# Kernel tuning notes

Measured on AMD Instinct MI355X. Metric: run time of the kernel, lower is better.

Reference implementation:

```python
import jax, jax.numpy as jnp
import numpy as np

B, S, H = 64, 2048, 1024
NEG = -1e10


def setup_inputs() -> dict:
    key = jax.random.key(0)
    k1, k2, k3, k4, k5, k6 = jax.random.split(key, 6)
    scale = 1.0 / np.sqrt(2 * H)
    return {
        "decoder_hidden": jax.random.normal(k1, (B, H), dtype=jnp.float32),
        "encoder_outputs": jax.random.normal(k2, (B, S, H), dtype=jnp.float32),
        "mask": jax.random.randint(k3, (B, S), 0, 2, dtype=jnp.int32),
        "W_attn": jax.random.normal(k4, (2 * H, H), dtype=jnp.float32) * scale,
        "b_attn": jax.random.normal(k5, (H,), dtype=jnp.float32) * scale,
        "v_w": jax.random.normal(k6, (H,), dtype=jnp.float32) * (1.0 / np.sqrt(H)),
    }


def reference(decoder_hidden, encoder_outputs, mask, W_attn, b_attn, v_w):
    # concat((dec_rep, enc), -1) @ W_attn == dec @ W_attn[:H] + enc @ W_attn[H:]
    Wd, We = W_attn[:H], W_attn[H:]
    dec_proj = decoder_hidden @ Wd            # [B, H]
    enc_proj = jnp.einsum('bsh,hk->bsk', encoder_outputs, We)  # [B, S, H]
    energy = jnp.tanh(dec_proj[:, None, :] + enc_proj + b_attn)  # [B, S, H]
    attention = jnp.einsum('bsh,h->bs', energy, v_w)             # [B, S]
    attention = jnp.where(mask == 1, NEG, attention)
    return jax.nn.softmax(attention, axis=1)
```

## Files before the change

### kernel.cpp

```cpp
#include <hip/hip_runtime.h>
#include <hip/hip_bf16.h>
#include <stdint.h>

#define HD   1024
#define BB   64
#define SS   2048
#define MT   (BB*SS)
#define NEGV -10000000000.0f

typedef __attribute__((ext_vector_type(8))) short bf16x8;
typedef __attribute__((ext_vector_type(4))) float f32x4;
typedef __attribute__((ext_vector_type(4))) int   i32x4;

__device__ __forceinline__ void gll16(const void* g, void* l) {
  __builtin_amdgcn_global_load_lds((const __attribute__((address_space(1))) void*)g,
                                   (__attribute__((address_space(3))) void*)l, 16, 0, 0);
}

__device__ __forceinline__ float tanh_fast(float x) {
  float e = __expf(2.0f * x);
  return 1.0f - 2.0f / (e + 1.0f);
}


__global__ void prep_we(const float* __restrict__ Wattn, __hip_bfloat16* __restrict__ out) {
  __shared__ float st[64][132];
  int tid = threadIdx.x;
  int nt = blockIdx.x >> 4, kc = blockIdx.x & 15;
  const float* src = Wattn + (size_t)(HD + kc*64)*HD + nt*128;
  #pragma unroll 4
  for (int i = 0; i < 32; ++i) {
    int s = i*256 + tid;
    int kk = s >> 7, nn = s & 127;
    st[kk][nn] = src[(size_t)kk*HD + nn];
  }
  __syncthreads();
  size_t base = (size_t)blockIdx.x * 8192;
  #pragma unroll 4
  for (int i = 0; i < 32; ++i) {
    int lin = i*256 + tid;
    int nl = lin >> 6, j = (lin >> 3) & 7, e = lin & 7;
    int kk = ((j ^ (nl & 7)) << 3) + e;
    out[base + lin] = __float2bfloat16(st[kk][nl]);
  }
}

__global__ void prep_E(const float* __restrict__ E, __hip_bfloat16* __restrict__ out) {
  int tid = threadIdx.x;
  int mt = blockIdx.x >> 4, kc = blockIdx.x & 15;
  const float* src = E + ((size_t)mt*128)*HD + kc*64;
  __hip_bfloat16* dst = out + (size_t)blockIdx.x * 8192;
  #pragma unroll
  for (int i = 0; i < 4; ++i) {
    int u = i*256 + tid;
    int ml = u >> 3, j = u & 7;
    int sk = ((j ^ (ml & 7)) << 3);
    const float* p = src + (size_t)ml*HD + sk;
    f32x4 v0 = *(const f32x4*)p;
    f32x4 v1 = *(const f32x4*)(p + 4);
    union { __hip_bfloat162 h[4]; i32x4 q; } cv;
    cv.h[0] = __float22bfloat162_rn(make_float2(v0.x, v0.y));
    cv.h[1] = __float22bfloat162_rn(make_float2(v0.z, v0.w));
    cv.h[2] = __float22bfloat162_rn(make_float2(v1.x, v1.y));
    cv.h[3] = __float22bfloat162_rn(make_float2(v1.z, v1.w));
    *(i32x4*)(dst + (size_t)u*8) = cv.q;
  }
}

__global__ void prep_dpb(const float* __restrict__ dec, const float* __restrict__ Wattn,
                         const float* __restrict__ battn, float* __restrict__ dpb) {
  __shared__ float red[4][64];
  int b = blockIdx.y, n0 = blockIdx.x*64;
  int nn = threadIdx.x & 63, kg = threadIdx.x >> 6;
  const float* wp = Wattn + (size_t)(kg*256)*HD + n0 + nn;
  const float* dp = dec + b*HD + kg*256;
  float acc = 0.0f;
  #pragma unroll 8
  for (int h = 0; h < 256; ++h) acc += dp[h] * wp[(size_t)h*HD];
  red[kg][nn] = acc;
  __syncthreads();
  if (threadIdx.x < 64) {
    int n = n0 + threadIdx.x;
    dpb[b*HD + n] = battn[n] + red[0][threadIdx.x] + red[1][threadIdx.x]
                             + red[2][threadIdx.x] + red[3][threadIdx.x];
  }
}

__device__ __forceinline__ void decode_bid(int bid, int& bm, int& bn) {
  int x = bid & 7, r = bid >> 3;
  bm = x*128 + (r >> 3);
  bn = r & 7;
}

__global__ void __launch_bounds__(256) gemm_fused_bf(
    const __hip_bfloat16* __restrict__ At, const __hip_bfloat16* __restrict__ Wt,
    const float* __restrict__ dpb, const float* __restrict__ vw,
    float* __restrict__ logits) {
  __shared__ __align__(16) short Al[128*64];
  __shared__ __align__(16) short Bl[128*64];
  __shared__ float red[128];

  int tid = threadIdx.x;
  int lane = tid & 63, wid = tid >> 6;
  int wm = wid & 1, wn = wid >> 1;
  int bm, bn; decode_bid(blockIdx.x, bm, bn);
  int m0 = bm << 7, n0 = bn << 7;
  int lane15 = lane & 15, kg = lane >> 4;

  f32x4 acc[4][4];
  #pragma unroll
  for (int a = 0; a < 4; ++a)
    #pragma unroll
    for (int c = 0; c < 4; ++c) acc[a][c] = (f32x4){0.f, 0.f, 0.f, 0.f};

  for (int kc = 0; kc < 16; ++kc) {
    const char* at = (const char*)At + ((size_t)(bm*16 + kc) * 8192) * 2;
    const char* bt = (const char*)Wt + ((size_t)(bn*16 + kc) * 8192) * 2;
    #pragma unroll
    for (int i = 0; i < 4; ++i) {
      int segbase = (wid*4 + i) * 64;
      gll16(at + (size_t)(segbase + lane)*16, (char*)Al + segbase*16);
      gll16(bt + (size_t)(segbase + lane)*16, (char*)Bl + segbase*16);
    }
    __syncthreads();
    #pragma unroll
    for (int kh = 0; kh < 2; ++kh) {
      bf16x8 af[4], bfr[4];
      #pragma unroll
      for (int mf = 0; mf < 4; ++mf) {
        int row = wm*64 + mf*16 + lane15;
        int jj = kh*4 + kg;
        af[mf] = *(const bf16x8*)&Al[row*64 + ((jj ^ (row & 7)) << 3)];
      }
      #pragma unroll
      for (int nf = 0; nf < 4; ++nf) {
        int nl = wn*64 + nf*16 + lane15;
        int jj = kh*4 + kg;
        bfr[nf] = *(const bf16x8*)&Bl[nl*64 + ((jj ^ (nl & 7)) << 3)];
      }
      #pragma unroll
      for (int mf = 0; mf < 4; ++mf)
        #pragma unroll
        for (int nf = 0; nf < 4; ++nf)
          acc[mf][nf] = __builtin_amdgcn_mfma_f32_16x16x32_bf16(af[mf], bfr[nf], acc[mf][nf], 0, 0, 0);
    }
    __syncthreads();
  }

  int bidx = m0 >> 11;
  float dpv[4], vwv[4];
  #pragma unroll
  for (int nf = 0; nf < 4; ++nf) {
    int n = n0 + wn*64 + nf*16 + lane15;
    dpv[nf] = dpb[bidx*HD + n];
    vwv[nf] = vw[n];
  }
  if (tid < 128) red[tid] = 0.0f;
  __syncthreads();
  #pragma unroll
  for (int mf = 0; mf < 4; ++mf) {
    #pragma unroll
    for (int r = 0; r < 4; ++r) {
      float s = 0.0f;
      #pragma unroll
      for (int nf = 0; nf < 4; ++nf) {
        float x = acc[mf][nf][r] + dpv[nf];
        s += tanh_fast(x) * vwv[nf];
      }
      s += __shfl_xor(s, 1); s += __shfl_xor(s, 2);
      s += __shfl_xor(s, 4); s += __shfl_xor(s, 8);
      if (lane15 == 0) atomicAdd(&red[wm*64 + mf*16 + kg*4 + r], s);
    }
  }
  __syncthreads();
  if (tid < 128) atomicAdd(&logits[m0 + tid], red[tid]);
}

__global__ void __launch_bounds__(256) gemm_fused_f32(
    const float* __restrict__ E, const __hip_bfloat16* __restrict__ Wt,
    const float* __restrict__ dpb, const float* __restrict__ vw,
    float* __restrict__ logits) {
  __shared__ __align__(16) short Al[128*72];
  __shared__ __align__(16) short Bl[128*64];
  __shared__ float red[128];

  int tid = threadIdx.x;
  int lane = tid & 63, wid = tid >> 6;
  int wm = wid & 1, wn = wid >> 1;
  int bm, bn; decode_bid(blockIdx.x, bm, bn);
  int m0 = bm << 7, n0 = bn << 7;
  int lane15 = lane & 15, kg = lane >> 4;

  f32x4 acc[4][4];
  #pragma unroll
  for (int a = 0; a < 4; ++a)
    #pragma unroll
    for (int c = 0; c < 4; ++c) acc[a][c] = (f32x4){0.f, 0.f, 0.f, 0.f};

  for (int kc = 0; kc < 16; ++kc) {
    const char* bt = (const char*)Wt + ((size_t)(bn*16 + kc) * 8192) * 2;
    #pragma unroll
    for (int i = 0; i < 4; ++i) {
      int segbase = (wid*4 + i) * 64;
      gll16(bt + (size_t)(segbase + lane)*16, (char*)Bl + segbase*16);
    }
    const float* Eg = E + (m0*HD + kc*64);
    #pragma unroll
    for (int i = 0; i < 8; ++i) {
      int s = i*256 + tid;
      int r = s >> 4, q = s & 15;
      f32x4 v = *(const f32x4*)(Eg + r*HD + q*4);
      union { __hip_bfloat162 h[2]; unsigned long long u; } cv;
      cv.h[0] = __float22bfloat162_rn(make_float2(v.x, v.y));
      cv.h[1] = __float22bfloat162_rn(make_float2(v.z, v.w));
      *(unsigned long long*)&Al[r*72 + q*4] = cv.u;
    }
    __syncthreads();
    #pragma unroll
    for (int kh = 0; kh < 2; ++kh) {
      bf16x8 af[4], bfr[4];
      #pragma unroll
      for (int mf = 0; mf < 4; ++mf) {
        int row = wm*64 + mf*16 + lane15;
        af[mf] = *(const bf16x8*)&Al[row*72 + kh*32 + kg*8];
      }
      #pragma unroll
      for (int nf = 0; nf < 4; ++nf) {
        int nl = wn*64 + nf*16 + lane15;
        int jj = kh*4 + kg;
        bfr[nf] = *(const bf16x8*)&Bl[nl*64 + ((jj ^ (nl & 7)) << 3)];
      }
      #pragma unroll
      for (int mf = 0; mf < 4; ++mf)
        #pragma unroll
        for (int nf = 0; nf < 4; ++nf)
          acc[mf][nf] = __builtin_amdgcn_mfma_f32_16x16x32_bf16(af[mf], bfr[nf], acc[mf][nf], 0, 0, 0);
    }
    __syncthreads();
  }

  int bidx = m0 >> 11;
  float dpv[4], vwv[4];
  #pragma unroll
  for (int nf = 0; nf < 4; ++nf) {
    int n = n0 + wn*64 + nf*16 + lane15;
    dpv[nf] = dpb[bidx*HD + n];
    vwv[nf] = vw[n];
  }
  if (tid < 128) red[tid] = 0.0f;
  __syncthreads();
  #pragma unroll
  for (int mf = 0; mf < 4; ++mf) {
    #pragma unroll
    for (int r = 0; r < 4; ++r) {
      float s = 0.0f;
      #pragma unroll
      for (int nf = 0; nf < 4; ++nf) {
        float x = acc[mf][nf][r] + dpv[nf];
        s += tanh_fast(x) * vwv[nf];
      }
      s += __shfl_xor(s, 1); s += __shfl_xor(s, 2);
      s += __shfl_xor(s, 4); s += __shfl_xor(s, 8);
      if (lane15 == 0) atomicAdd(&red[wm*64 + mf*16 + kg*4 + r], s);
    }
  }
  __syncthreads();
  if (tid < 128) atomicAdd(&logits[m0 + tid], red[tid]);
}

__global__ void softmax_k(const float* __restrict__ logits, const int* __restrict__ mask,
                          float* __restrict__ out) {
  __shared__ float smax[4];
  __shared__ float ssum[4];
  int tid = threadIdx.x, lane = tid & 63, wid = tid >> 6;
  int b = blockIdx.x;
  const float* lg = logits + b*SS;
  const int*   mk = mask   + b*SS;
  f32x4 l0 = *(const f32x4*)(lg + tid*8);
  f32x4 l1 = *(const f32x4*)(lg + tid*8 + 4);
  i32x4 q0 = *(const i32x4*)(mk + tid*8);
  i32x4 q1 = *(const i32x4*)(mk + tid*8 + 4);
  float v[8];
  v[0] = (q0.x == 1) ? NEGV : l0.x;  v[1] = (q0.y == 1) ? NEGV : l0.y;
  v[2] = (q0.z == 1) ? NEGV : l0.z;  v[3] = (q0.w == 1) ? NEGV : l0.w;
  v[4] = (q1.x == 1) ? NEGV : l1.x;  v[5] = (q1.y == 1) ? NEGV : l1.y;
  v[6] = (q1.z == 1) ? NEGV : l1.z;  v[7] = (q1.w == 1) ? NEGV : l1.w;
  float mx = v[0];
  #pragma unroll
  for (int i = 1; i < 8; ++i) mx = fmaxf(mx, v[i]);
  #pragma unroll
  for (int m = 1; m <= 32; m <<= 1) mx = fmaxf(mx, __shfl_xor(mx, m));
  if (lane == 0) smax[wid] = mx;
  __syncthreads();
  mx = fmaxf(fmaxf(smax[0], smax[1]), fmaxf(smax[2], smax[3]));
  float s = 0.0f;
  #pragma unroll
  for (int i = 0; i < 8; ++i) { v[i] = __expf(v[i] - mx); s += v[i]; }
  #pragma unroll
  for (int m = 1; m <= 32; m <<= 1) s += __shfl_xor(s, m);
  if (lane == 0) ssum[wid] = s;
  __syncthreads();
  s = ssum[0] + ssum[1] + ssum[2] + ssum[3];
  float inv = 1.0f / s;
  f32x4 o0 = {v[0]*inv, v[1]*inv, v[2]*inv, v[3]*inv};
  f32x4 o1 = {v[4]*inv, v[5]*inv, v[6]*inv, v[7]*inv};
  *(f32x4*)(out + b*SS + tid*8)     = o0;
  *(f32x4*)(out + b*SS + tid*8 + 4) = o1;
}

extern "C" void kernel_launch(void* const* d_in, const int* in_sizes, int n_in,
                              void* d_out, int out_size, void* d_ws, size_t ws_size,
                              hipStream_t stream) {
  const float* dec   = (const float*)d_in[0];
  const float* enc   = (const float*)d_in[1];
  const int*   mask  = (const int*)  d_in[2];
  const float* Wattn = (const float*)d_in[3];
  const float* battn = (const float*)d_in[4];
  const float* vw    = (const float*)d_in[5];
  float* out = (float*)d_out;

  const size_t EBF_BYTES = (size_t)MT * HD * 2;
  const size_t FAST_NEED = EBF_BYTES + (2u<<20) + (256u<<10) + (512u<<10);

  char* ws = (char*)d_ws;
  if (ws_size >= FAST_NEED) {
    __hip_bfloat16* ebf = (__hip_bfloat16*)ws;
    __hip_bfloat16* wet = (__hip_bfloat16*)(ws + EBF_BYTES);
    float* dpb    = (float*)(ws + EBF_BYTES + (2u<<20));
    float* logits = (float*)(ws + EBF_BYTES + (2u<<20) + (256u<<10));

    prep_E <<<16384, 256, 0, stream>>>(enc, ebf);
    prep_we<<<128, 256, 0, stream>>>(Wattn, wet);
    prep_dpb<<<dim3(16, 64), 256, 0, stream>>>(dec, Wattn, battn, dpb);
    hipMemsetAsync(logits, 0, (size_t)MT*sizeof(float), stream);
    gemm_fused_bf<<<8192, 256, 0, stream>>>(ebf, wet, dpb, vw, logits);
    softmax_k<<<BB, 256, 0, stream>>>(logits, mask, out);
  } else {
    __hip_bfloat16* wet = (__hip_bfloat16*)ws;
    float* dpb    = (float*)(ws + (2u<<20));
    float* logits = (float*)(ws + (2u<<20) + (256u<<10));

    prep_we<<<128, 256, 0, stream>>>(Wattn, wet);
    prep_dpb<<<dim3(16, 64), 256, 0, stream>>>(dec, Wattn, battn, dpb);
    hipMemsetAsync(logits, 0, (size_t)MT*sizeof(float), stream);
    gemm_fused_f32<<<8192, 256, 0, stream>>>(enc, wet, dpb, vw, logits);
    softmax_k<<<BB, 256, 0, stream>>>(logits, mask, out);
  }
}
```

Measured before the change: 1.200 ms.

## Replace bf16 fused GEMM with 256x256 tile, 8-wave, phased double-buffered pipeline

Swaps the 128x128 single-buffered bf16 GEMM for a 256x256 tile kernel with 8 waves. Global-to-LDS loads are double-buffered across 128 KB of LDS and interleaved with four MFMA phases per K step, using explicit waitcnt, barriers and setprio. The goal is to hide load latency behind compute and halve global traffic per FLOP through larger tiles. tanh_fast also switches its divide to a hardware reciprocal. The cost is heavy LDS use that limits occupancy and fragile hand-tuned synchronisation.

```diff
diff --git a/kernel.cpp b/kernel.cpp
--- a/kernel.cpp
+++ b/kernel.cpp
@@ -19,7 +19,7 @@
 
 __device__ __forceinline__ float tanh_fast(float x) {
   float e = __expf(2.0f * x);
-  return 1.0f - 2.0f / (e + 1.0f);
+  return 1.0f - 2.0f * __builtin_amdgcn_rcpf(e + 1.0f);
 }
 
 
@@ -86,94 +86,162 @@
   }
 }
 
+__global__ void __launch_bounds__(512, 2) gemm_fused_8ph(
+    const __hip_bfloat16* __restrict__ At, const __hip_bfloat16* __restrict__ Wt,
+    const float* __restrict__ dpb, const float* __restrict__ vw,
+    float* __restrict__ logits) {
+  __shared__ __align__(16) char lds[131072];
+
+  int tid = threadIdx.x;
+  int lane = tid & 63, wid = tid >> 6;
+  int wm = wid & 1, wn = wid >> 1;
+  int lane15 = lane & 15, kg = lane >> 4;
+
+  int x = blockIdx.x & 7, r = blockIdx.x >> 3;
+  int bm = x*64 + (r >> 2);
+  int bn = r & 3;
+
+  f32x4 acc[2][2][4][2];
+  #pragma unroll
+  for (int i = 0; i < 2; ++i)
+    #pragma unroll
+    for (int j = 0; j < 2; ++j)
+      #pragma unroll
+      for (int k = 0; k < 4; ++k)
+        #pragma unroll
+        for (int l = 0; l < 2; ++l)
+          acc[i][j][k][l] = (f32x4){0.f, 0.f, 0.f, 0.f};
+
+  bf16x8 af[4][2], bfr[2][2];
+
+  auto stage = [&](int op, int h, int t) {
+    const char* g = op ? ((const char*)Wt + (((size_t)(bn*2 + h)*16 + t) << 14))
+                       : ((const char*)At + (((size_t)(bm*2 + h)*16 + t) << 14));
+    char* l = lds + ((t & 1) << 16) + (op << 15) + (h << 14);
+    gll16(g + (size_t)(wid*64 + lane)*16,     l + wid*1024);
+    gll16(g + (size_t)((8+wid)*64 + lane)*16, l + (8+wid)*1024);
+  };
+  auto readA = [&](int hr, int t) {
+    const char* b = lds + ((t & 1) << 16) + (hr << 14);
+    #pragma unroll
+    for (int mf = 0; mf < 4; ++mf) {
+      int ll = wm*64 + mf*16 + lane15;
+      const char* rp = b + ll*128;
+      int sw = (ll & 7) << 4;
+      af[mf][0] = *(const bf16x8*)(rp + ((kg << 4) ^ sw));
+      af[mf][1] = *(const bf16x8*)(rp + (((4 + kg) << 4) ^ sw));
+    }
+  };
+  auto readB = [&](int hc, int t) {
+    const char* b = lds + ((t & 1) << 16) + 32768 + (hc << 14);
+    #pragma unroll
+    for (int nf = 0; nf < 2; ++nf) {
+      int ll = wn*32 + nf*16 + lane15;
+      const char* rp = b + ll*128;
+      int sw = (ll & 7) << 4;
+      bfr[nf][0] = *(const bf16x8*)(rp + ((kg << 4) ^ sw));
+      bfr[nf][1] = *(const bf16x8*)(rp + (((4 + kg) << 4) ^ sw));
+    }
+  };
+
+#define MFMA_PH(HR, HC) do {                                                   \
+    __builtin_amdgcn_s_setprio(1);                                             \
+    _Pragma("unroll")                                                          \
+    for (int kk = 0; kk < 2; ++kk)                                             \
+      _Pragma("unroll")                                                        \
+      for (int mf = 0; mf < 4; ++mf)                                           \
+        _Pragma("unroll")                                                      \
+        for (int nf = 0; nf < 2; ++nf)                                         \
+          acc[HR][HC][mf][nf] = __builtin_amdgcn_mfma_f32_16x16x32_bf16(       \
+              af[mf][kk], bfr[nf][kk], acc[HR][HC][mf][nf], 0, 0, 0);          \
+    __builtin_amdgcn_s_setprio(0);                                             \
+    __builtin_amdgcn_sched_barrier(0);                                         \
+  } while (0)
+
+#define PH_SYNC() do {                                                         \
+    __builtin_amdgcn_s_barrier();                                              \
+    asm volatile("s_waitcnt lgkmcnt(0)");                                      \
+    __builtin_amdgcn_sched_barrier(0);                                         \
+  } while (0)
+
+  stage(0, 0, 0); stage(1, 1, 0); stage(0, 1, 0); stage(1, 0, 0);
+  stage(0, 0, 1); stage(1, 1, 1); stage(0, 1, 1);
+  asm volatile("s_waitcnt vmcnt(6)" ::: "memory");
+  __builtin_amdgcn_s_barrier();
+
+  #pragma unroll 2
+  for (int t = 0; t < 16; ++t) {
+    readA(0, t); readB(0, t);
+    if (t + 1 < 16) stage(1, 0, t + 1);
+    asm volatile("s_waitcnt lgkmcnt(8)");
+    PH_SYNC();
+    MFMA_PH(0, 0);
+    __builtin_amdgcn_s_barrier();
+
+    readB(1, t);
+    if (t + 2 < 16) stage(0, 0, t + 2);
+    PH_SYNC();
+    MFMA_PH(0, 1);
+    __builtin_amdgcn_s_barrier();
+
+    readA(1, t);
+    if (t + 2 < 16) stage(1, 1, t + 2);
+    PH_SYNC();
+    MFMA_PH(1, 1);
+    __builtin_amdgcn_s_barrier();
+
+    readB(0, t);
+    if (t + 2 < 16) stage(0, 1, t + 2);
+    PH_SYNC();
+    MFMA_PH(1, 0);
+    if (t < 14) asm volatile("s_waitcnt vmcnt(6)" ::: "memory");
+    else        asm volatile("s_waitcnt vmcnt(0)" ::: "memory");
+    __builtin_amdgcn_s_barrier();
+  }
+#undef MFMA_PH
+#undef PH_SYNC
+
+  __syncthreads();
+  float* red = (float*)lds;
+  if (tid < 256) red[tid] = 0.0f;
+  __syncthreads();
+
+  int m0 = bm << 8, n0 = bn << 8;
+  int bidx = m0 >> 11;
+  float dpv[2][2], vwv[2][2];
+  #pragma unroll
+  for (int hc = 0; hc < 2; ++hc)
+    #pragma unroll
+    for (int nf = 0; nf < 2; ++nf) {
+      int n = n0 + hc*128 + wn*32 + nf*16 + lane15;
+      dpv[hc][nf] = dpb[bidx*HD + n];
+      vwv[hc][nf] = vw[n];
+    }
+
+  #pragma unroll
+  for (int hr = 0; hr < 2; ++hr)
+    #pragma unroll
+    for (int mf = 0; mf < 4; ++mf)
+      #pragma unroll
+      for (int rr = 0; rr < 4; ++rr) {
+        float s = 0.0f;
+        #pragma unroll
+        for (int hc = 0; hc < 2; ++hc)
+          #pragma unroll
+          for (int nf = 0; nf < 2; ++nf)
+            s += tanh_fast(acc[hr][hc][mf][nf][rr] + dpv[hc][nf]) * vwv[hc][nf];
+        s += __shfl_xor(s, 1); s += __shfl_xor(s, 2);
+        s += __shfl_xor(s, 4); s += __shfl_xor(s, 8);
+        if (lane15 == 0) atomicAdd(&red[hr*128 + wm*64 + mf*16 + kg*4 + rr], s);
+      }
+  __syncthreads();
+  if (tid < 256) atomicAdd(&logits[m0 + tid], red[tid]);
+}
+
 __device__ __forceinline__ void decode_bid(int bid, int& bm, int& bn) {
   int x = bid & 7, r = bid >> 3;
   bm = x*128 + (r >> 3);
   bn = r & 7;
-}
-
-__global__ void __launch_bounds__(256) gemm_fused_bf(
-    const __hip_bfloat16* __restrict__ At, const __hip_bfloat16* __restrict__ Wt,
-    const float* __restrict__ dpb, const float* __restrict__ vw,
-    float* __restrict__ logits) {
-  __shared__ __align__(16) short Al[128*64];
-  __shared__ __align__(16) short Bl[128*64];
-  __shared__ float red[128];
-
-  int tid = threadIdx.x;
-  int lane = tid & 63, wid = tid >> 6;
-  int wm = wid & 1, wn = wid >> 1;
-  int bm, bn; decode_bid(blockIdx.x, bm, bn);
-  int m0 = bm << 7, n0 = bn << 7;
-  int lane15 = lane & 15, kg = lane >> 4;
-
-  f32x4 acc[4][4];
-  #pragma unroll
-  for (int a = 0; a < 4; ++a)
-    #pragma unroll
-    for (int c = 0; c < 4; ++c) acc[a][c] = (f32x4){0.f, 0.f, 0.f, 0.f};
-
-  for (int kc = 0; kc < 16; ++kc) {
-    const char* at = (const char*)At + ((size_t)(bm*16 + kc) * 8192) * 2;
-    const char* bt = (const char*)Wt + ((size_t)(bn*16 + kc) * 8192) * 2;
-    #pragma unroll
-    for (int i = 0; i < 4; ++i) {
-      int segbase = (wid*4 + i) * 64;
-      gll16(at + (size_t)(segbase + lane)*16, (char*)Al + segbase*16);
-      gll16(bt + (size_t)(segbase + lane)*16, (char*)Bl + segbase*16);
-    }
-    __syncthreads();
-    #pragma unroll
-    for (int kh = 0; kh < 2; ++kh) {
-      bf16x8 af[4], bfr[4];
-      #pragma unroll
-      for (int mf = 0; mf < 4; ++mf) {
-        int row = wm*64 + mf*16 + lane15;
-        int jj = kh*4 + kg;
-        af[mf] = *(const bf16x8*)&Al[row*64 + ((jj ^ (row & 7)) << 3)];
-      }
-      #pragma unroll
-      for (int nf = 0; nf < 4; ++nf) {
-        int nl = wn*64 + nf*16 + lane15;
-        int jj = kh*4 + kg;
-        bfr[nf] = *(const bf16x8*)&Bl[nl*64 + ((jj ^ (nl & 7)) << 3)];
-      }
-      #pragma unroll
-      for (int mf = 0; mf < 4; ++mf)
-        #pragma unroll
-        for (int nf = 0; nf < 4; ++nf)
-          acc[mf][nf] = __builtin_amdgcn_mfma_f32_16x16x32_bf16(af[mf], bfr[nf], acc[mf][nf], 0, 0, 0);
-    }
-    __syncthreads();
-  }
-
-  int bidx = m0 >> 11;
-  float dpv[4], vwv[4];
-  #pragma unroll
-  for (int nf = 0; nf < 4; ++nf) {
-    int n = n0 + wn*64 + nf*16 + lane15;
-    dpv[nf] = dpb[bidx*HD + n];
-    vwv[nf] = vw[n];
-  }
-  if (tid < 128) red[tid] = 0.0f;
-  __syncthreads();
-  #pragma unroll
-  for (int mf = 0; mf < 4; ++mf) {
-    #pragma unroll
-    for (int r = 0; r < 4; ++r) {
-      float s = 0.0f;
-      #pragma unroll
-      for (int nf = 0; nf < 4; ++nf) {
-        float x = acc[mf][nf][r] + dpv[nf];
-        s += tanh_fast(x) * vwv[nf];
-      }
-      s += __shfl_xor(s, 1); s += __shfl_xor(s, 2);
-      s += __shfl_xor(s, 4); s += __shfl_xor(s, 8);
-      if (lane15 == 0) atomicAdd(&red[wm*64 + mf*16 + kg*4 + r], s);
-    }
-  }
-  __syncthreads();
-  if (tid < 128) atomicAdd(&logits[m0 + tid], red[tid]);
 }
 
 __global__ void __launch_bounds__(256) gemm_fused_f32(
@@ -333,7 +401,7 @@
     prep_we<<<128, 256, 0, stream>>>(Wattn, wet);
     prep_dpb<<<dim3(16, 64), 256, 0, stream>>>(dec, Wattn, battn, dpb);
     hipMemsetAsync(logits, 0, (size_t)MT*sizeof(float), stream);
-    gemm_fused_bf<<<8192, 256, 0, stream>>>(ebf, wet, dpb, vw, logits);
+    gemm_fused_8ph<<<2048, 512, 0, stream>>>(ebf, wet, dpb, vw, logits);
     softmax_k<<<BB, 256, 0, stream>>>(logits, mask, out);
   } else {
     __hip_bfloat16* wet = (__hip_bfloat16*)ws;
```

After: 1.032 ms. 1.16x faster.
